# Kernel optimization log

Hardware: AMD Instinct MI355X
Metric: run time of the kernel (lower is better)

## Reference

```python
import jax, jax.numpy as jnp
import numpy as np

N_NODES = 10000


def sage_conv(x, src, dst, W_l, b_l, W_r):
    # PyG SAGEConv with mean aggregation:
    #   out = lin_l(mean_{j in N(i)} x_j) + lin_r(x_i)
    msgs = x[src]  # [E, d] gather of source-node features
    agg = jax.ops.segment_sum(msgs, dst, num_segments=N_NODES)  # [N, d]
    cnt = jax.ops.segment_sum(jnp.ones((src.shape[0],), x.dtype), dst,
                              num_segments=N_NODES)  # [N]
    mean = agg / jnp.maximum(cnt, 1.0)[:, None]  # zero rows for isolated nodes
    return mean @ W_l + b_l + x @ W_r


def setup_inputs() -> dict:
    key = jax.random.key(0)
    ks = jax.random.split(key, 12)
    in_c, hid, out_c = 128, 128, 128
    x = jax.random.normal(ks[0], (N_NODES, in_c), dtype=jnp.float32)
    edge_index = jax.random.randint(ks[1], (2, 640000), 0, N_NODES, dtype=jnp.int64)

    def lin(k, fan_in, fan_out):
        s = 1.0 / np.sqrt(fan_in)
        return jax.random.uniform(k, (fan_in, fan_out), jnp.float32, -s, s)

    params = {
        'W1_l': lin(ks[2], in_c, hid), 'b1_l': jnp.zeros((hid,), jnp.float32),
        'W1_r': lin(ks[3], in_c, hid),
        'W2_l': lin(ks[4], hid, hid), 'b2_l': jnp.zeros((hid,), jnp.float32),
        'W2_r': lin(ks[5], hid, hid),
        'W3_l': lin(ks[6], hid, out_c), 'b3_l': jnp.zeros((out_c,), jnp.float32),
        'W3_r': lin(ks[7], hid, out_c),
        'W_cls': lin(ks[8], out_c, 1), 'b_cls': jnp.zeros((1,), jnp.float32),
    }
    return {'x': x, 'edge_index': edge_index, **params}


def reference(x, edge_index, W1_l, b1_l, W1_r, W2_l, b2_l, W2_r,
              W3_l, b3_l, W3_r, W_cls, b_cls):
    src, dst = edge_index[0], edge_index[1]
    h = jax.nn.relu(sage_conv(x, src, dst, W1_l, b1_l, W1_r))
    # dropout is identity in eval mode
    h = jax.nn.relu(sage_conv(h, src, dst, W2_l, b2_l, W2_r))
    h = jax.nn.relu(sage_conv(h, src, dst, W3_l, b3_l, W3_r))
    logits = h @ W_cls + b_cls  # [N, 1]
    return jax.nn.sigmoid(logits)[:, 0]  # [N]
```

## Files before the change

### kernel.cpp

```cpp
#include <hip/hip_runtime.h>
#include <hip/hip_fp16.h>
#include <math.h>

#define N_NODES 10000
#define D 128
#define NCOPY 8

typedef unsigned int uint_t;
typedef unsigned short ushort_t;
typedef __attribute__((ext_vector_type(8))) _Float16 f16x8;
typedef __attribute__((ext_vector_type(4))) float f32x4;

#define MFMA16(a, b, c) __builtin_amdgcn_mfma_f32_16x16x32_f16((a), (b), (c), 0, 0, 0)

__device__ inline uint_t pack_h2(float lo, float hi) {
    __half2 h = __floats2half2_rn(lo, hi);
    return *(uint_t*)&h;
}
__device__ inline void acc_h8(uint4 v, float4& aA, float4& aB) {
    float2 f;
    f = __half22float2(*(__half2*)&v.x); aA.x += f.x; aA.y += f.y;
    f = __half22float2(*(__half2*)&v.y); aA.z += f.x; aA.w += f.y;
    f = __half22float2(*(__half2*)&v.z); aB.x += f.x; aB.y += f.y;
    f = __half22float2(*(__half2*)&v.w); aB.z += f.x; aB.w += f.y;
}

__global__ void prep_kernel(const float* __restrict__ x, __half* __restrict__ xm,
                            const float* __restrict__ W1l, const float* __restrict__ W1r,
                            const float* __restrict__ W2l, const float* __restrict__ W2r,
                            const float* __restrict__ W3l, const float* __restrict__ W3r,
                            __half* __restrict__ WT,
                            uint4* __restrict__ deg8z, int n8, int nz16, int nwt) {
    int i = blockIdx.x * blockDim.x + threadIdx.x;
    if (i < nz16) deg8z[i] = make_uint4(0u, 0u, 0u, 0u);
    if (i < n8) {
        const float4* p = (const float4*)x + (size_t)i * 2;
        float4 a = p[0], b = p[1];
        uint4 o;
        o.x = pack_h2(a.x, a.y); o.y = pack_h2(a.z, a.w);
        o.z = pack_h2(b.x, b.y); o.w = pack_h2(b.z, b.w);
        ((uint4*)xm)[i] = o;
    }
    if (i < nwt) {
        int m = i >> 14, idx = i & 16383;
        int n = idx >> 7, k = idx & 127;
        const float* Wm = (m == 0) ? W1l : (m == 1) ? W1r : (m == 2) ? W2l
                        : (m == 3) ? W2r : (m == 4) ? W3l : W3r;
        WT[i] = __float2half_rn(Wm[k * D + n]);
    }
}

__global__ void rank_kernel(const int* __restrict__ dst, int E,
                            int* __restrict__ deg8, int* __restrict__ pos) {
    int i = blockIdx.x * blockDim.x + threadIdx.x;
    if (i < E) {
        int c = blockIdx.x & (NCOPY - 1);
        pos[i] = atomicAdd(&deg8[c * N_NODES + dst[i]], 1);
    }
}

__global__ void sumdeg_kernel(const int* __restrict__ deg8, int* __restrict__ tot, int n) {
    int i = blockIdx.x * blockDim.x + threadIdx.x;
    if (i < n) {
        int s = 0;
#pragma unroll
        for (int c = 0; c < NCOPY; ++c) s += deg8[c * N_NODES + i];
        tot[i] = s;
    }
}

#define SCAN_PER 10
__global__ __launch_bounds__(1024) void scan_kernel(const int* __restrict__ tot,
                                                    int* __restrict__ offsets, int n) {
    __shared__ int wsum[16];
    __shared__ int wpre[16];
    int tid = threadIdx.x;
    int lane = tid & 63, wid = tid >> 6;
    int base = tid * SCAN_PER;
    int loc[SCAN_PER];
    int s = 0;
#pragma unroll
    for (int q = 0; q < SCAN_PER; ++q) {
        int idx = base + q;
        int v = (idx < n) ? tot[idx] : 0;
        s += v;
        loc[q] = s;
    }
    int mysum = s;
#pragma unroll
    for (int off = 1; off < 64; off <<= 1) {
        int t = __shfl_up(s, off, 64);
        if (lane >= off) s += t;
    }
    if (lane == 63) wsum[wid] = s;
    __syncthreads();
    if (wid == 0 && lane < 16) {
        int v = wsum[lane];
        int ss = v;
#pragma unroll
        for (int off = 1; off < 16; off <<= 1) {
            int t = __shfl_up(ss, off, 16);
            if ((lane & 15) >= off) ss += t;
        }
        wpre[lane] = ss - v;
    }
    __syncthreads();
    int thread_excl = wpre[wid] + (s - mysum);
#pragma unroll
    for (int q = 0; q < SCAN_PER; ++q) {
        int idx = base + q;
        if (idx < n) offsets[idx + 1] = thread_excl + loc[q];
    }
    if (tid == 0) offsets[0] = 0;
}

__global__ void base8_kernel(const int* __restrict__ deg8, const int* __restrict__ offsets,
                             int* __restrict__ base8, int n) {
    int i = blockIdx.x * blockDim.x + threadIdx.x;
    if (i < n) {
        int run = offsets[i];
#pragma unroll
        for (int c = 0; c < NCOPY; ++c) {
            base8[c * N_NODES + i] = run;
            run += deg8[c * N_NODES + i];
        }
    }
}

__global__ void csr_write_kernel(const int* __restrict__ src, const int* __restrict__ dst,
                                 const int* __restrict__ pos, int E,
                                 const int* __restrict__ base8, int* __restrict__ csr_src) {
    int i = blockIdx.x * blockDim.x + threadIdx.x;
    if (i < E) {
        int c = (i >> 8) & (NCOPY - 1);
        csr_src[base8[c * N_NODES + dst[i]] + pos[i]] = src[i];
    }
}

__global__ __launch_bounds__(256) void aggregate_kernel(const __half* __restrict__ h16,
                                                        const int* __restrict__ offsets,
                                                        const int* __restrict__ csr_src,
                                                        __half* __restrict__ mean16) {
    __shared__ float tmp[3][16][8];
    int node = blockIdx.x;
    int tid = threadIdx.x;
    int g = tid >> 4;
    int fl = tid & 15;
    int beg = offsets[node], end = offsets[node + 1];
    float4 aA = make_float4(0.f, 0.f, 0.f, 0.f);
    float4 aB = make_float4(0.f, 0.f, 0.f, 0.f);
    for (int e = beg + g; e < end; e += 16) {
        int s = csr_src[e];
        uint4 v = *(const uint4*)&h16[s * D + fl * 8];
        acc_h8(v, aA, aB);
    }
    aA.x += __shfl_xor(aA.x, 16, 64); aA.y += __shfl_xor(aA.y, 16, 64);
    aA.z += __shfl_xor(aA.z, 16, 64); aA.w += __shfl_xor(aA.w, 16, 64);
    aB.x += __shfl_xor(aB.x, 16, 64); aB.y += __shfl_xor(aB.y, 16, 64);
    aB.z += __shfl_xor(aB.z, 16, 64); aB.w += __shfl_xor(aB.w, 16, 64);
    aA.x += __shfl_xor(aA.x, 32, 64); aA.y += __shfl_xor(aA.y, 32, 64);
    aA.z += __shfl_xor(aA.z, 32, 64); aA.w += __shfl_xor(aA.w, 32, 64);
    aB.x += __shfl_xor(aB.x, 32, 64); aB.y += __shfl_xor(aB.y, 32, 64);
    aB.z += __shfl_xor(aB.z, 32, 64); aB.w += __shfl_xor(aB.w, 32, 64);
    int wv = tid >> 6;
    int lane = tid & 63;
    if (wv > 0 && lane < 16) {
        *(float4*)&tmp[wv - 1][lane][0] = aA;
        *(float4*)&tmp[wv - 1][lane][4] = aB;
    }
    __syncthreads();
    if (tid < 16) {
#pragma unroll
        for (int w = 0; w < 3; ++w) {
            float4 oA = *(const float4*)&tmp[w][tid][0];
            float4 oB = *(const float4*)&tmp[w][tid][4];
            aA.x += oA.x; aA.y += oA.y; aA.z += oA.z; aA.w += oA.w;
            aB.x += oB.x; aB.y += oB.y; aB.z += oB.z; aB.w += oB.w;
        }
        int cnt = end - beg;
        float inv = (cnt > 0) ? (1.0f / (float)cnt) : 0.f;
        uint4 o;
        o.x = pack_h2(aA.x * inv, aA.y * inv);
        o.y = pack_h2(aA.z * inv, aA.w * inv);
        o.z = pack_h2(aB.x * inv, aB.y * inv);
        o.w = pack_h2(aB.z * inv, aB.w * inv);
        *(uint4*)&mean16[node * D + tid * 8] = o;
    }
}

__global__ __launch_bounds__(128) void lin_mfma_kernel(
        const __half* __restrict__ A1, const __half* __restrict__ A2,
        const __half* __restrict__ BT1, const __half* __restrict__ BT2,
        const float* __restrict__ bias, __half* __restrict__ out16,
        const float* __restrict__ Wc, const float* __restrict__ bcls,
        float* __restrict__ cls) {
    __shared__ float pl[2][16];
    int r0 = blockIdx.x * 16;
    int w  = (int)threadIdx.x >> 6;
    int l  = (int)threadIdx.x & 63;
    int lr = l & 15;
    int kg = l >> 4;

    const __half* a1p = A1 + (r0 + lr) * D + kg * 8;
    const __half* a2p = A2 + (r0 + lr) * D + kg * 8;
    f16x8 a1f[4], a2f[4];
#pragma unroll
    for (int ko = 0; ko < 4; ++ko) {
        a1f[ko] = *(const f16x8*)(a1p + ko * 32);
        a2f[ko] = *(const f16x8*)(a2p + ko * 32);
    }

    float p0 = 0.f, p1 = 0.f, p2 = 0.f, p3 = 0.f;

#pragma unroll
    for (int ct = 0; ct < 4; ++ct) {
        int c = w * 64 + ct * 16 + lr;
        const __half* b1p = BT1 + c * D + kg * 8;
        const __half* b2p = BT2 + c * D + kg * 8;
        f32x4 acc = {0.f, 0.f, 0.f, 0.f};
#pragma unroll
        for (int ko = 0; ko < 4; ++ko)
            acc = MFMA16(a1f[ko], *(const f16x8*)(b1p + ko * 32), acc);
#pragma unroll
        for (int ko = 0; ko < 4; ++ko)
            acc = MFMA16(a2f[ko], *(const f16x8*)(b2p + ko * 32), acc);

        float bcol = bias[c];
        float v0 = fmaxf(acc[0] + bcol, 0.f);
        float v1 = fmaxf(acc[1] + bcol, 0.f);
        float v2 = fmaxf(acc[2] + bcol, 0.f);
        float v3 = fmaxf(acc[3] + bcol, 0.f);
        if (Wc) {
            float wc = Wc[c];
            p0 += v0 * wc; p1 += v1 * wc; p2 += v2 * wc; p3 += v3 * wc;
        } else {
            int rbase = (r0 + kg * 4) * D + c;
            out16[rbase]         = __float2half_rn(v0);
            out16[rbase + D]     = __float2half_rn(v1);
            out16[rbase + 2 * D] = __float2half_rn(v2);
            out16[rbase + 3 * D] = __float2half_rn(v3);
        }
    }

    if (Wc) {
#pragma unroll
        for (int off = 1; off <= 8; off <<= 1) {
            p0 += __shfl_xor(p0, off, 64);
            p1 += __shfl_xor(p1, off, 64);
            p2 += __shfl_xor(p2, off, 64);
            p3 += __shfl_xor(p3, off, 64);
        }
        if (lr == 0) {
            pl[w][kg * 4 + 0] = p0;
            pl[w][kg * 4 + 1] = p1;
            pl[w][kg * 4 + 2] = p2;
            pl[w][kg * 4 + 3] = p3;
        }
        __syncthreads();
        if (threadIdx.x < 16) {
            float s = pl[0][threadIdx.x] + pl[1][threadIdx.x] + bcls[0];
            cls[r0 + threadIdx.x] = 1.0f / (1.0f + expf(-s));
        }
    }
}

extern "C" void kernel_launch(void* const* d_in, const int* in_sizes, int n_in,
                              void* d_out, int out_size, void* d_ws, size_t ws_size,
                              hipStream_t stream) {
    const float* x   = (const float*)d_in[0];
    const int* eidx  = (const int*)d_in[1];
    int E = in_sizes[1] / 2;
    const int* src = eidx;
    const int* dst = eidx + E;
    const float* W1l = (const float*)d_in[2];
    const float* b1  = (const float*)d_in[3];
    const float* W1r = (const float*)d_in[4];
    const float* W2l = (const float*)d_in[5];
    const float* b2  = (const float*)d_in[6];
    const float* W2r = (const float*)d_in[7];
    const float* W3l = (const float*)d_in[8];
    const float* b3  = (const float*)d_in[9];
    const float* W3r = (const float*)d_in[10];
    const float* Wc  = (const float*)d_in[11];
    const float* bc  = (const float*)d_in[12];
    float* out = (float*)d_out;

    char* p = (char*)d_ws;
    int* deg8      = (int*)p;   p += (size_t)NCOPY * N_NODES * 4;
    int* base8     = (int*)p;   p += (size_t)NCOPY * N_NODES * 4;
    int* offsets   = (int*)p;   p += 40960;
    int* tot       = (int*)p;   p += 40960;
    int* csr_src   = (int*)p;   p += (size_t)E * 4;
    int* pos       = (int*)p;   p += (size_t)E * 4;
    __half* mean16 = (__half*)p; p += (size_t)N_NODES * D * 2;
    __half* xm     = (__half*)p; p += (size_t)N_NODES * D * 2;
    __half* m1     = (__half*)p; p += (size_t)N_NODES * D * 2;
    __half* m2     = (__half*)p; p += (size_t)N_NODES * D * 2;
    __half* WT     = (__half*)p; p += (size_t)6 * D * D * 2;

    int n8  = N_NODES * D / 8;
    int nz16 = (NCOPY * N_NODES * 4) / 16;
    int nwt = 6 * D * D;
    prep_kernel<<<(n8 + 255) / 256, 256, 0, stream>>>(
        x, xm, W1l, W1r, W2l, W2r, W3l, W3r, WT, (uint4*)deg8, n8, nz16, nwt);

    int eb = (E + 255) / 256;
    int nb = (N_NODES + 255) / 256;
    rank_kernel<<<eb, 256, 0, stream>>>(dst, E, deg8, pos);
    sumdeg_kernel<<<nb, 256, 0, stream>>>(deg8, tot, N_NODES);
    scan_kernel<<<1, 1024, 0, stream>>>(tot, offsets, N_NODES);
    base8_kernel<<<nb, 256, 0, stream>>>(deg8, offsets, base8, N_NODES);
    csr_write_kernel<<<eb, 256, 0, stream>>>(src, dst, pos, E, base8, csr_src);

    int lin_grid = N_NODES / 16;

    aggregate_kernel<<<N_NODES, 256, 0, stream>>>(xm, offsets, csr_src, mean16);
    lin_mfma_kernel<<<lin_grid, 128, 0, stream>>>(
        mean16, xm, WT, WT + D * D, b1, m1,
        (const float*)nullptr, (const float*)nullptr, (float*)nullptr);
    aggregate_kernel<<<N_NODES, 256, 0, stream>>>(m1, offsets, csr_src, mean16);
    lin_mfma_kernel<<<lin_grid, 128, 0, stream>>>(
        mean16, m1, WT + 2 * D * D, WT + 3 * D * D, b2, m2,
        (const float*)nullptr, (const float*)nullptr, (float*)nullptr);
    aggregate_kernel<<<N_NODES, 256, 0, stream>>>(m2, offsets, csr_src, mean16);
    lin_mfma_kernel<<<lin_grid, 128, 0, stream>>>(
        mean16, m2, WT + 4 * D * D, WT + 5 * D * D, b3, (__half*)nullptr,
        Wc, bc, out);
}
```

Before: 138.7 us.

## Widen degree copies, stage scan through LDS, and unroll aggregation gathers

Raises the number of per-copy degree counters from 8 to 16 so fewer blocks contend on the same atomics during ranking. The single-block scan now loads and stores through shared memory with coalesced global access instead of strided per-thread access. The aggregation loop handles two edges per iteration with separate accumulators, which increases memory-level parallelism for the feature gathers. The cost is more memory to zero and sum for the degree copies, plus a 40KB LDS buffer in the scan.

```diff
diff --git a/kernel.cpp b/kernel.cpp
--- a/kernel.cpp
+++ b/kernel.cpp
@@ -4,10 +4,9 @@
 
 #define N_NODES 10000
 #define D 128
-#define NCOPY 8
+#define NCOPY 16
 
 typedef unsigned int uint_t;
-typedef unsigned short ushort_t;
 typedef __attribute__((ext_vector_type(8))) _Float16 f16x8;
 typedef __attribute__((ext_vector_type(4))) float f32x4;
 
@@ -30,9 +29,9 @@
                             const float* __restrict__ W2l, const float* __restrict__ W2r,
                             const float* __restrict__ W3l, const float* __restrict__ W3r,
                             __half* __restrict__ WT,
-                            uint4* __restrict__ deg8z, int n8, int nz16, int nwt) {
-    int i = blockIdx.x * blockDim.x + threadIdx.x;
-    if (i < nz16) deg8z[i] = make_uint4(0u, 0u, 0u, 0u);
+                            uint4* __restrict__ degz, int n8, int nz16, int nwt) {
+    int i = blockIdx.x * blockDim.x + threadIdx.x;
+    if (i < nz16) degz[i] = make_uint4(0u, 0u, 0u, 0u);
     if (i < n8) {
         const float4* p = (const float4*)x + (size_t)i * 2;
         float4 a = p[0], b = p[1];
@@ -51,39 +50,45 @@
 }
 
 __global__ void rank_kernel(const int* __restrict__ dst, int E,
-                            int* __restrict__ deg8, int* __restrict__ pos) {
+                            int* __restrict__ degN, int* __restrict__ pos) {
     int i = blockIdx.x * blockDim.x + threadIdx.x;
     if (i < E) {
         int c = blockIdx.x & (NCOPY - 1);
-        pos[i] = atomicAdd(&deg8[c * N_NODES + dst[i]], 1);
-    }
-}
-
-__global__ void sumdeg_kernel(const int* __restrict__ deg8, int* __restrict__ tot, int n) {
+        pos[i] = atomicAdd(&degN[c * N_NODES + dst[i]], 1);
+    }
+}
+
+__global__ void sumdeg_kernel(const int* __restrict__ degN, int* __restrict__ tot, int n) {
     int i = blockIdx.x * blockDim.x + threadIdx.x;
     if (i < n) {
         int s = 0;
 #pragma unroll
-        for (int c = 0; c < NCOPY; ++c) s += deg8[c * N_NODES + i];
+        for (int c = 0; c < NCOPY; ++c) s += degN[c * N_NODES + i];
         tot[i] = s;
     }
 }
 
 #define SCAN_PER 10
+#define SCAN_N 10240
 __global__ __launch_bounds__(1024) void scan_kernel(const int* __restrict__ tot,
                                                     int* __restrict__ offsets, int n) {
+    __shared__ int buf[SCAN_N];
     __shared__ int wsum[16];
     __shared__ int wpre[16];
     int tid = threadIdx.x;
     int lane = tid & 63, wid = tid >> 6;
+#pragma unroll
+    for (int q = 0; q < SCAN_PER; ++q) {
+        int idx = q * 1024 + tid;
+        buf[idx] = (idx < n) ? tot[idx] : 0;
+    }
+    __syncthreads();
     int base = tid * SCAN_PER;
     int loc[SCAN_PER];
     int s = 0;
 #pragma unroll
     for (int q = 0; q < SCAN_PER; ++q) {
-        int idx = base + q;
-        int v = (idx < n) ? tot[idx] : 0;
-        s += v;
+        s += buf[base + q];
         loc[q] = s;
     }
     int mysum = s;
@@ -107,33 +112,36 @@
     __syncthreads();
     int thread_excl = wpre[wid] + (s - mysum);
 #pragma unroll
+    for (int q = 0; q < SCAN_PER; ++q) buf[base + q] = thread_excl + loc[q];
+    __syncthreads();
+#pragma unroll
     for (int q = 0; q < SCAN_PER; ++q) {
-        int idx = base + q;
-        if (idx < n) offsets[idx + 1] = thread_excl + loc[q];
+        int idx = q * 1024 + tid;
+        if (idx < n) offsets[idx + 1] = buf[idx];
     }
     if (tid == 0) offsets[0] = 0;
 }
 
-__global__ void base8_kernel(const int* __restrict__ deg8, const int* __restrict__ offsets,
-                             int* __restrict__ base8, int n) {
+__global__ void baseN_kernel(const int* __restrict__ degN, const int* __restrict__ offsets,
+                             int* __restrict__ baseN, int n) {
     int i = blockIdx.x * blockDim.x + threadIdx.x;
     if (i < n) {
         int run = offsets[i];
 #pragma unroll
         for (int c = 0; c < NCOPY; ++c) {
-            base8[c * N_NODES + i] = run;
-            run += deg8[c * N_NODES + i];
+            baseN[c * N_NODES + i] = run;
+            run += degN[c * N_NODES + i];
         }
     }
 }
 
 __global__ void csr_write_kernel(const int* __restrict__ src, const int* __restrict__ dst,
                                  const int* __restrict__ pos, int E,
-                                 const int* __restrict__ base8, int* __restrict__ csr_src) {
+                                 const int* __restrict__ baseN, int* __restrict__ csr_src) {
     int i = blockIdx.x * blockDim.x + threadIdx.x;
     if (i < E) {
         int c = (i >> 8) & (NCOPY - 1);
-        csr_src[base8[c * N_NODES + dst[i]] + pos[i]] = src[i];
+        csr_src[baseN[c * N_NODES + dst[i]] + pos[i]] = src[i];
     }
 }
 
@@ -149,11 +157,24 @@
     int beg = offsets[node], end = offsets[node + 1];
     float4 aA = make_float4(0.f, 0.f, 0.f, 0.f);
     float4 aB = make_float4(0.f, 0.f, 0.f, 0.f);
-    for (int e = beg + g; e < end; e += 16) {
-        int s = csr_src[e];
-        uint4 v = *(const uint4*)&h16[s * D + fl * 8];
-        acc_h8(v, aA, aB);
-    }
+    float4 cA = make_float4(0.f, 0.f, 0.f, 0.f);
+    float4 cB = make_float4(0.f, 0.f, 0.f, 0.f);
+    int e = beg + g;
+    for (; e + 16 < end; e += 32) {
+        int s0 = csr_src[e];
+        int s1 = csr_src[e + 16];
+        uint4 v0 = *(const uint4*)&h16[s0 * D + fl * 8];
+        uint4 v1 = *(const uint4*)&h16[s1 * D + fl * 8];
+        acc_h8(v0, aA, aB);
+        acc_h8(v1, cA, cB);
+    }
+    if (e < end) {
+        int s0 = csr_src[e];
+        uint4 v0 = *(const uint4*)&h16[s0 * D + fl * 8];
+        acc_h8(v0, aA, aB);
+    }
+    aA.x += cA.x; aA.y += cA.y; aA.z += cA.z; aA.w += cA.w;
+    aB.x += cB.x; aB.y += cB.y; aB.z += cB.z; aB.w += cB.w;
     aA.x += __shfl_xor(aA.x, 16, 64); aA.y += __shfl_xor(aA.y, 16, 64);
     aA.z += __shfl_xor(aA.z, 16, 64); aA.w += __shfl_xor(aA.w, 16, 64);
     aB.x += __shfl_xor(aB.x, 16, 64); aB.y += __shfl_xor(aB.y, 16, 64);
@@ -286,8 +307,8 @@
     float* out = (float*)d_out;
 
     char* p = (char*)d_ws;
-    int* deg8      = (int*)p;   p += (size_t)NCOPY * N_NODES * 4;
-    int* base8     = (int*)p;   p += (size_t)NCOPY * N_NODES * 4;
+    int* degN      = (int*)p;   p += (size_t)NCOPY * N_NODES * 4;
+    int* baseN     = (int*)p;   p += (size_t)NCOPY * N_NODES * 4;
     int* offsets   = (int*)p;   p += 40960;
     int* tot       = (int*)p;   p += 40960;
     int* csr_src   = (int*)p;   p += (size_t)E * 4;
@@ -302,15 +323,15 @@
     int nz16 = (NCOPY * N_NODES * 4) / 16;
     int nwt = 6 * D * D;
     prep_kernel<<<(n8 + 255) / 256, 256, 0, stream>>>(
-        x, xm, W1l, W1r, W2l, W2r, W3l, W3r, WT, (uint4*)deg8, n8, nz16, nwt);
+        x, xm, W1l, W1r, W2l, W2r, W3l, W3r, WT, (uint4*)degN, n8, nz16, nwt);
 
     int eb = (E + 255) / 256;
     int nb = (N_NODES + 255) / 256;
-    rank_kernel<<<eb, 256, 0, stream>>>(dst, E, deg8, pos);
-    sumdeg_kernel<<<nb, 256, 0, stream>>>(deg8, tot, N_NODES);
+    rank_kernel<<<eb, 256, 0, stream>>>(dst, E, degN, pos);
+    sumdeg_kernel<<<nb, 256, 0, stream>>>(degN, tot, N_NODES);
     scan_kernel<<<1, 1024, 0, stream>>>(tot, offsets, N_NODES);
-    base8_kernel<<<nb, 256, 0, stream>>>(deg8, offsets, base8, N_NODES);
-    csr_write_kernel<<<eb, 256, 0, stream>>>(src, dst, pos, E, base8, csr_src);
+    baseN_kernel<<<nb, 256, 0, stream>>>(degN, offsets, baseN, N_NODES);
+    csr_write_kernel<<<eb, 256, 0, stream>>>(src, dst, pos, E, baseN, csr_src);
 
     int lin_grid = N_NODES / 16;
 
```

Result: faster. 129.4 us, median of 3 (-6.7%).
